# Kernel tuning notes

Measured on AMD Instinct MI355X. Metric: run time of the kernel, lower is better.

## Reference

```python
import jax, jax.numpy as jnp
import numpy as np

N, F_IN, F_OUT = 8192, 512, 256
NEG_BIG = -9e15


def setup_inputs() -> dict:
    key = jax.random.key(0)
    k1, k2, k3, k4, k5 = jax.random.split(key, 5)
    h = jax.random.normal(k1, (N, F_IN), dtype=jnp.float32)
    adj = jax.random.randint(k2, (N, N), 0, 2, dtype=jnp.int32)
    W = jax.random.normal(k3, (F_IN, F_OUT), dtype=jnp.float32) / np.sqrt(F_IN)
    bW = jnp.zeros((F_OUT,), dtype=jnp.float32)
    a1 = jax.random.normal(k4, (F_OUT,), dtype=jnp.float32) / np.sqrt(2 * F_OUT)
    a2 = jax.random.normal(k5, (F_OUT,), dtype=jnp.float32) / np.sqrt(2 * F_OUT)
    ba = jnp.zeros((), dtype=jnp.float32)
    return {"h": h, "adj": adj, "W": W, "bW": bW, "a1": a1, "a2": a2, "ba": ba}


def reference(h, adj, W, bW, a1, a2, ba):
    # Wh: [N, F_OUT]
    Wh = h @ W + bW
    # a([Wh_i ; Wh_j]) + b == (Wh_i . a1) + (Wh_j . a2) + b  (rank-1 decomposition,
    # avoids the O(N^2 * 2F) repeat/cat tensor the torch code materializes)
    f1 = Wh @ a1  # [N]
    f2 = Wh @ a2  # [N]
    e = jax.nn.leaky_relu(f1[:, None] + f2[None, :] + ba, negative_slope=0.2)
    e = jnp.where(adj > 0, e, NEG_BIG)
    attention = jax.nn.softmax(e, axis=1)  # dropout = identity (eval mode)
    return attention @ Wh
```

## Files before the change

### kernel.cpp

```cpp
#include <hip/hip_runtime.h>

typedef __bf16 bf16;
typedef __attribute__((ext_vector_type(4))) float f32x4;
typedef __attribute__((ext_vector_type(8))) __bf16 bf16x8;
typedef __attribute__((ext_vector_type(4))) __bf16 bf16x4;
typedef __attribute__((ext_vector_type(4))) int i32x4;

#define NN 8192
#define FI 512
#define FO 256
#define NSPLIT 4
#define JCHUNK (NN / NSPLIT)

__global__ __launch_bounds__(256) void k1_gemm(
    const float* __restrict__ h, const float* __restrict__ W,
    const float* __restrict__ bW, const float* __restrict__ a1,
    const float* __restrict__ a2, bf16* __restrict__ whb,
    float* __restrict__ f1, float* __restrict__ f2) {
  __shared__ float As[16][68];
  __shared__ float Bs[16][72];
  const int t = threadIdx.x;
  const int bi = blockIdx.x, bj = blockIdx.y;
  const int tx = t & 15, ty = t >> 4;
  const int lr = t >> 2, lc = (t & 3) * 4;
  const int wr = t >> 4, wc = (t & 15) * 4;
  float acc[4][4] = {};
  const float* hrow = h + (size_t)(bi * 64 + lr) * FI;
  for (int kt = 0; kt < FI / 16; ++kt) {
    f32x4 hv = *(const f32x4*)(hrow + kt * 16 + lc);
    f32x4 wv = *(const f32x4*)(W + (size_t)(kt * 16 + wr) * FO + bj * 64 + wc);
    __syncthreads();
    As[lc + 0][lr] = hv.x; As[lc + 1][lr] = hv.y;
    As[lc + 2][lr] = hv.z; As[lc + 3][lr] = hv.w;
    *(f32x4*)&Bs[wr][wc] = wv;
    __syncthreads();
#pragma unroll
    for (int k = 0; k < 16; ++k) {
      f32x4 av = *(const f32x4*)&As[k][ty * 4];
      f32x4 bv = *(const f32x4*)&Bs[k][tx * 4];
#pragma unroll
      for (int r = 0; r < 4; ++r)
#pragma unroll
        for (int cc = 0; cc < 4; ++cc)
          acc[r][cc] += av[r] * bv[cc];
    }
  }
  const int i0 = bi * 64 + ty * 4;
  const int n0 = bj * 64 + tx * 4;
  float f1p[4] = {}, f2p[4] = {};
#pragma unroll
  for (int r = 0; r < 4; ++r) {
    const int i = i0 + r;
#pragma unroll
    for (int cc = 0; cc < 4; ++cc) {
      const int n = n0 + cc;
      float wh = acc[r][cc] + bW[n];
      whb[(size_t)(i >> 5) * (FO * 32) + n * 32 + (i & 31)] = (bf16)wh;
      f1p[r] += wh * a1[n];
      f2p[r] += wh * a2[n];
    }
  }
#pragma unroll
  for (int m = 1; m < 16; m <<= 1) {
#pragma unroll
    for (int r = 0; r < 4; ++r) {
      f1p[r] += __shfl_xor(f1p[r], m);
      f2p[r] += __shfl_xor(f2p[r], m);
    }
  }
  if (tx == 0) {
#pragma unroll
    for (int r = 0; r < 4; ++r) {
      atomicAdd(&f1[i0 + r], f1p[r]);
      atomicAdd(&f2[i0 + r], f2p[r]);
    }
  }
}

__global__ __launch_bounds__(256) void k3_max(const float* __restrict__ f2,
                                              float* __restrict__ Mstar) {
  __shared__ float red[4];
  const int t = threadIdx.x;
  float m = -1e30f;
  for (int i = t; i < NN; i += 256) m = fmaxf(m, f2[i]);
#pragma unroll
  for (int d = 1; d < 64; d <<= 1) m = fmaxf(m, __shfl_xor(m, d));
  if ((t & 63) == 0) red[t >> 6] = m;
  __syncthreads();
  if (t == 0) *Mstar = fmaxf(fmaxf(red[0], red[1]), fmaxf(red[2], red[3]));
}

__global__ __launch_bounds__(256) void k4_attn(
    const int* __restrict__ adj, const bf16* __restrict__ whb,
    const float* __restrict__ f1, const float* __restrict__ f2,
    const float* __restrict__ Mstar, const float* __restrict__ ba_p,
    float* __restrict__ acc_part, float* __restrict__ l_part) {
  __shared__ bf16 Pl[32 * 40];
  __shared__ bf16 Bl[256 * 40];
  const int t = threadIdx.x;
  const int lane = t & 63, w = t >> 6;
  const int rb = blockIdx.x, s = blockIdx.y;
  const int i0 = rb * 32;
  const int rloc = t >> 3;
  const int jj = (t & 7) * 4;
  const int m16 = lane & 15, q = lane >> 4;

  const float ba = *ba_p;
  const float Ms = *Mstar;
  const float ci = f1[i0 + rloc] + ba;
  float sh = ci + Ms;
  sh = fmaxf(sh, 0.2f * sh);

  const f32x4 z4 = {0.f, 0.f, 0.f, 0.f};
  f32x4 acc0[4], acc1[4];
#pragma unroll
  for (int cc = 0; cc < 4; ++cc) { acc0[cc] = z4; acc1[cc] = z4; }
  float lreg = 0.f;

  const int* adjrow = adj + (size_t)(i0 + rloc) * NN;

  for (int kt = 0; kt < JCHUNK / 32; ++kt) {
    const int j0 = s * JCHUNK + kt * 32;
    i32x4 a4 = *(const i32x4*)(adjrow + j0 + jj);
    f32x4 s4 = *(const f32x4*)(f2 + j0 + jj);
    const size_t jt_base = (size_t)(j0 >> 5) * (FO * 32);
    bf16x8 bstg[4];
#pragma unroll
    for (int u = 0; u < 4; ++u)
      bstg[u] = *(const bf16x8*)(whb + jt_base + (size_t)(t + 256 * u) * 8);
    float pv[4];
#pragma unroll
    for (int x = 0; x < 4; ++x) {
      float arg = ci + s4[x];
      float e = fmaxf(arg, 0.2f * arg);
      pv[x] = (a4[x] > 0) ? __expf(e - sh) : 0.f;
    }
    lreg += pv[0] + pv[1] + pv[2] + pv[3];
    __syncthreads();
    bf16x4 pb = {(bf16)pv[0], (bf16)pv[1], (bf16)pv[2], (bf16)pv[3]};
    *(bf16x4*)&Pl[rloc * 40 + jj] = pb;
#pragma unroll
    for (int u = 0; u < 4; ++u) {
      const int tt = t + 256 * u;
      *(bf16x8*)&Bl[(tt >> 2) * 40 + (tt & 3) * 8] = bstg[u];
    }
    __syncthreads();
    bf16x8 af0 = *(const bf16x8*)&Pl[m16 * 40 + q * 8];
    bf16x8 af1 = *(const bf16x8*)&Pl[(16 + m16) * 40 + q * 8];
#pragma unroll
    for (int cc = 0; cc < 4; ++cc) {
      bf16x8 bfr = *(const bf16x8*)&Bl[((w * 4 + cc) * 16 + m16) * 40 + q * 8];
      acc0[cc] = __builtin_amdgcn_mfma_f32_16x16x32_bf16(af0, bfr, acc0[cc], 0, 0, 0);
      acc1[cc] = __builtin_amdgcn_mfma_f32_16x16x32_bf16(af1, bfr, acc1[cc], 0, 0, 0);
    }
  }
  lreg += __shfl_xor(lreg, 1);
  lreg += __shfl_xor(lreg, 2);
  lreg += __shfl_xor(lreg, 4);
  if ((t & 7) == 0) l_part[(size_t)s * NN + i0 + rloc] = lreg;
  float* ap = acc_part + (size_t)s * ((size_t)NN * FO);
#pragma unroll
  for (int cc = 0; cc < 4; ++cc) {
    const int n = (w * 4 + cc) * 16 + m16;
#pragma unroll
    for (int reg = 0; reg < 4; ++reg) {
      const int r0 = i0 + q * 4 + reg;
      ap[(size_t)r0 * FO + n] = acc0[cc][reg];
      ap[(size_t)(r0 + 16) * FO + n] = acc1[cc][reg];
    }
  }
}

__global__ __launch_bounds__(256) void k5_reduce(
    const float* __restrict__ accp, const float* __restrict__ lp,
    float* __restrict__ out) {
  const int idx = blockIdx.x * 256 + threadIdx.x;
  const int i = idx >> 6, n4 = (idx & 63) * 4;
  f32x4 sum = {0.f, 0.f, 0.f, 0.f};
  float l = 0.f;
#pragma unroll
  for (int s = 0; s < NSPLIT; ++s) {
    sum += *(const f32x4*)&accp[(size_t)s * ((size_t)NN * FO) + (size_t)i * FO + n4];
    l += lp[s * NN + i];
  }
  const float rl = 1.0f / l;
  f32x4 o = sum * rl;
  *(f32x4*)&out[(size_t)i * FO + n4] = o;
}

extern "C" void kernel_launch(void* const* d_in, const int* in_sizes, int n_in,
                              void* d_out, int out_size, void* d_ws, size_t ws_size,
                              hipStream_t stream) {
  const float* h  = (const float*)d_in[0];
  const int*   adj = (const int*)d_in[1];
  const float* W  = (const float*)d_in[2];
  const float* bW = (const float*)d_in[3];
  const float* a1 = (const float*)d_in[4];
  const float* a2 = (const float*)d_in[5];
  const float* ba = (const float*)d_in[6];
  float* out = (float*)d_out;

  char* ws = (char*)d_ws;
  bf16* whb  = (bf16*)ws;
  float* f1  = (float*)(ws + 4u * 1024 * 1024);
  float* f2  = (float*)(ws + 4u * 1024 * 1024 + 32 * 1024);
  float* Mst = (float*)(ws + 4u * 1024 * 1024 + 64 * 1024);
  float* accp = (float*)(ws + 4u * 1024 * 1024 + 64 * 1024 + 256);
  float* lp   = accp + (size_t)NSPLIT * NN * FO;

  hipMemsetAsync(f1, 0, 64 * 1024, stream);

  k1_gemm<<<dim3(NN / 64, FO / 64), 256, 0, stream>>>(h, W, bW, a1, a2, whb, f1, f2);
  k3_max<<<1, 256, 0, stream>>>(f2, Mst);
  k4_attn<<<dim3(NN / 32, NSPLIT), 256, 0, stream>>>(adj, whb, f1, f2, Mst, ba, accp, lp);
  k5_reduce<<<(NN * FO / 4) / 256, 256, 0, stream>>>(accp, lp, out);
}
```

Measured before the change: 488.3 us.

## Pack adjacency to bitmask, use split-bf16 MFMA projection GEMM, enlarge attention row tile

Adds a pre-pass that packs the int32 adjacency matrix into a 1-bit mask. The attention kernel then reads the mask instead of the adjacency and processes 64 rows per block. It also loads Wh fragments straight from global memory into registers rather than staging them through LDS. The feature GEMM becomes an MFMA kernel that approximates fp32 with hi/lo bf16 splits of h and a pre-transposed W. The full adjacency is still read once in the pack pass, so the gain depends on cutting the attention kernel's traffic and LDS synchronisation, at the cost of extra launches and a larger workspace.

Result: no change. 481.4 us (-1.4%).

```diff
diff --git a/kernel.cpp b/kernel.cpp
--- a/kernel.cpp
+++ b/kernel.cpp
@@ -12,68 +12,126 @@
 #define NSPLIT 4
 #define JCHUNK (NN / NSPLIT)
 
+__global__ __launch_bounds__(256) void k0_pack(const int* __restrict__ adj,
+                                               unsigned* __restrict__ mask) {
+  const int gid = blockIdx.x * 256 + threadIdx.x;
+  const int* p = adj + (size_t)gid * 32;
+  unsigned m = 0;
+#pragma unroll
+  for (int u = 0; u < 8; ++u) {
+    i32x4 v = *(const i32x4*)(p + u * 4);
+    m |= (unsigned)(v.x > 0) << (u * 4 + 0);
+    m |= (unsigned)(v.y > 0) << (u * 4 + 1);
+    m |= (unsigned)(v.z > 0) << (u * 4 + 2);
+    m |= (unsigned)(v.w > 0) << (u * 4 + 3);
+  }
+  mask[gid] = m;
+}
+
+__global__ __launch_bounds__(256) void kw_split(const float* __restrict__ W,
+                                                bf16* __restrict__ wth,
+                                                bf16* __restrict__ wtl) {
+  const int idx = blockIdx.x * 256 + threadIdx.x;
+  const int k = idx >> 8, n = idx & 255;
+  float x = W[idx];
+  bf16 hi = (bf16)x;
+  wth[(size_t)n * FI + k] = hi;
+  wtl[(size_t)n * FI + k] = (bf16)(x - (float)hi);
+}
+
 __global__ __launch_bounds__(256) void k1_gemm(
-    const float* __restrict__ h, const float* __restrict__ W,
-    const float* __restrict__ bW, const float* __restrict__ a1,
-    const float* __restrict__ a2, bf16* __restrict__ whb,
-    float* __restrict__ f1, float* __restrict__ f2) {
-  __shared__ float As[16][68];
-  __shared__ float Bs[16][72];
+    const float* __restrict__ h, const bf16* __restrict__ wth,
+    const bf16* __restrict__ wtl, const float* __restrict__ bW,
+    const float* __restrict__ a1, const float* __restrict__ a2,
+    bf16* __restrict__ whb, float* __restrict__ f1, float* __restrict__ f2) {
+  __shared__ bf16 Ah[32 * 40];
+  __shared__ bf16 Al[32 * 40];
   const int t = threadIdx.x;
+  const int lane = t & 63, w = t >> 6;
+  const int m16 = lane & 15, q = lane >> 4;
   const int bi = blockIdx.x, bj = blockIdx.y;
-  const int tx = t & 15, ty = t >> 4;
-  const int lr = t >> 2, lc = (t & 3) * 4;
-  const int wr = t >> 4, wc = (t & 15) * 4;
-  float acc[4][4] = {};
-  const float* hrow = h + (size_t)(bi * 64 + lr) * FI;
-  for (int kt = 0; kt < FI / 16; ++kt) {
-    f32x4 hv = *(const f32x4*)(hrow + kt * 16 + lc);
-    f32x4 wv = *(const f32x4*)(W + (size_t)(kt * 16 + wr) * FO + bj * 64 + wc);
-    __syncthreads();
-    As[lc + 0][lr] = hv.x; As[lc + 1][lr] = hv.y;
-    As[lc + 2][lr] = hv.z; As[lc + 3][lr] = hv.w;
-    *(f32x4*)&Bs[wr][wc] = wv;
-    __syncthreads();
-#pragma unroll
-    for (int k = 0; k < 16; ++k) {
-      f32x4 av = *(const f32x4*)&As[k][ty * 4];
-      f32x4 bv = *(const f32x4*)&Bs[k][tx * 4];
-#pragma unroll
-      for (int r = 0; r < 4; ++r)
-#pragma unroll
-        for (int cc = 0; cc < 4; ++cc)
-          acc[r][cc] += av[r] * bv[cc];
-    }
-  }
-  const int i0 = bi * 64 + ty * 4;
-  const int n0 = bj * 64 + tx * 4;
-  float f1p[4] = {}, f2p[4] = {};
-#pragma unroll
-  for (int r = 0; r < 4; ++r) {
-    const int i = i0 + r;
-#pragma unroll
-    for (int cc = 0; cc < 4; ++cc) {
-      const int n = n0 + cc;
-      float wh = acc[r][cc] + bW[n];
-      whb[(size_t)(i >> 5) * (FO * 32) + n * 32 + (i & 31)] = (bf16)wh;
-      f1p[r] += wh * a1[n];
-      f2p[r] += wh * a2[n];
+  const int i0 = bi * 32;
+  const int n0 = bj * 128 + w * 32;
+  const int srow = t >> 3, skoff = (t & 7) * 4;
+
+  const f32x4 z4 = {0.f, 0.f, 0.f, 0.f};
+  f32x4 acc[2][2];
+#pragma unroll
+  for (int mt = 0; mt < 2; ++mt)
+#pragma unroll
+    for (int nt = 0; nt < 2; ++nt) acc[mt][nt] = z4;
+
+  const float* hrow = h + (size_t)(i0 + srow) * FI + skoff;
+
+  for (int kt = 0; kt < FI / 32; ++kt) {
+    f32x4 hv = *(const f32x4*)(hrow + kt * 32);
+    bf16x8 bh[2], bl[2];
+#pragma unroll
+    for (int nt = 0; nt < 2; ++nt) {
+      const size_t woff = (size_t)(n0 + nt * 16 + m16) * FI + kt * 32 + q * 8;
+      bh[nt] = *(const bf16x8*)(wth + woff);
+      bl[nt] = *(const bf16x8*)(wtl + woff);
+    }
+    bf16x4 hh, hl;
+#pragma unroll
+    for (int x = 0; x < 4; ++x) {
+      float v = hv[x];
+      bf16 hi = (bf16)v;
+      hh[x] = hi;
+      hl[x] = (bf16)(v - (float)hi);
+    }
+    __syncthreads();
+    *(bf16x4*)&Ah[srow * 40 + skoff] = hh;
+    *(bf16x4*)&Al[srow * 40 + skoff] = hl;
+    __syncthreads();
+#pragma unroll
+    for (int mt = 0; mt < 2; ++mt) {
+      bf16x8 ah = *(const bf16x8*)&Ah[(mt * 16 + m16) * 40 + q * 8];
+      bf16x8 al = *(const bf16x8*)&Al[(mt * 16 + m16) * 40 + q * 8];
+#pragma unroll
+      for (int nt = 0; nt < 2; ++nt) {
+        acc[mt][nt] = __builtin_amdgcn_mfma_f32_16x16x32_bf16(ah, bh[nt], acc[mt][nt], 0, 0, 0);
+        acc[mt][nt] = __builtin_amdgcn_mfma_f32_16x16x32_bf16(al, bh[nt], acc[mt][nt], 0, 0, 0);
+        acc[mt][nt] = __builtin_amdgcn_mfma_f32_16x16x32_bf16(ah, bl[nt], acc[mt][nt], 0, 0, 0);
+      }
+    }
+  }
+  float f1p[2][4] = {}, f2p[2][4] = {};
+#pragma unroll
+  for (int nt = 0; nt < 2; ++nt) {
+    const int n = n0 + nt * 16 + m16;
+    const float bw = bW[n], av1 = a1[n], av2 = a2[n];
+#pragma unroll
+    for (int mt = 0; mt < 2; ++mt) {
+#pragma unroll
+      for (int reg = 0; reg < 4; ++reg) {
+        float wh = acc[mt][nt][reg] + bw;
+        const int il = mt * 16 + q * 4 + reg;
+        whb[(size_t)bi * (FO * 32) + n * 32 + il] = (bf16)wh;
+        f1p[mt][reg] += wh * av1;
+        f2p[mt][reg] += wh * av2;
+      }
     }
   }
 #pragma unroll
   for (int m = 1; m < 16; m <<= 1) {
 #pragma unroll
-    for (int r = 0; r < 4; ++r) {
-      f1p[r] += __shfl_xor(f1p[r], m);
-      f2p[r] += __shfl_xor(f2p[r], m);
-    }
-  }
-  if (tx == 0) {
-#pragma unroll
-    for (int r = 0; r < 4; ++r) {
-      atomicAdd(&f1[i0 + r], f1p[r]);
-      atomicAdd(&f2[i0 + r], f2p[r]);
-    }
+    for (int mt = 0; mt < 2; ++mt)
+#pragma unroll
+      for (int reg = 0; reg < 4; ++reg) {
+        f1p[mt][reg] += __shfl_xor(f1p[mt][reg], m);
+        f2p[mt][reg] += __shfl_xor(f2p[mt][reg], m);
+      }
+  }
+  if (m16 == 0) {
+#pragma unroll
+    for (int mt = 0; mt < 2; ++mt)
+#pragma unroll
+      for (int reg = 0; reg < 4; ++reg) {
+        const int i = i0 + mt * 16 + q * 4 + reg;
+        atomicAdd(&f1[i], f1p[mt][reg]);
+        atomicAdd(&f2[i], f2p[mt][reg]);
+      }
   }
 }
 
@@ -91,19 +149,18 @@
 }
 
 __global__ __launch_bounds__(256) void k4_attn(
-    const int* __restrict__ adj, const bf16* __restrict__ whb,
+    const unsigned* __restrict__ mask, const bf16* __restrict__ whb,
     const float* __restrict__ f1, const float* __restrict__ f2,
     const float* __restrict__ Mstar, const float* __restrict__ ba_p,
     float* __restrict__ acc_part, float* __restrict__ l_part) {
-  __shared__ bf16 Pl[32 * 40];
-  __shared__ bf16 Bl[256 * 40];
+  __shared__ bf16 Pl[64 * 40];
   const int t = threadIdx.x;
   const int lane = t & 63, w = t >> 6;
+  const int m16 = lane & 15, q = lane >> 4;
   const int rb = blockIdx.x, s = blockIdx.y;
-  const int i0 = rb * 32;
-  const int rloc = t >> 3;
-  const int jj = (t & 7) * 4;
-  const int m16 = lane & 15, q = lane >> 4;
+  const int i0 = rb * 64;
+  const int rloc = t >> 2;
+  const int jj = (t & 3) * 8;
 
   const float ba = *ba_p;
   const float Ms = *Mstar;
@@ -112,61 +169,69 @@
   sh = fmaxf(sh, 0.2f * sh);
 
   const f32x4 z4 = {0.f, 0.f, 0.f, 0.f};
-  f32x4 acc0[4], acc1[4];
-#pragma unroll
-  for (int cc = 0; cc < 4; ++cc) { acc0[cc] = z4; acc1[cc] = z4; }
+  f32x4 acc[4][4];
+#pragma unroll
+  for (int mt = 0; mt < 4; ++mt)
+#pragma unroll
+    for (int cc = 0; cc < 4; ++cc) acc[mt][cc] = z4;
   float lreg = 0.f;
 
-  const int* adjrow = adj + (size_t)(i0 + rloc) * NN;
+  const unsigned* mrow = mask + (size_t)(i0 + rloc) * (NN / 32);
+  const int sbase = s * JCHUNK;
 
   for (int kt = 0; kt < JCHUNK / 32; ++kt) {
-    const int j0 = s * JCHUNK + kt * 32;
-    i32x4 a4 = *(const i32x4*)(adjrow + j0 + jj);
-    f32x4 s4 = *(const f32x4*)(f2 + j0 + jj);
-    const size_t jt_base = (size_t)(j0 >> 5) * (FO * 32);
-    bf16x8 bstg[4];
-#pragma unroll
-    for (int u = 0; u < 4; ++u)
-      bstg[u] = *(const bf16x8*)(whb + jt_base + (size_t)(t + 256 * u) * 8);
-    float pv[4];
+    const int j0 = sbase + kt * 32;
+    const unsigned mw = mrow[j0 >> 5];
+    f32x4 s4a = *(const f32x4*)(f2 + j0 + jj);
+    f32x4 s4b = *(const f32x4*)(f2 + j0 + jj + 4);
+    const size_t bbase = (size_t)(j0 >> 5) * (FO * 32) + q * 8;
+    bf16x8 bfr[4];
+#pragma unroll
+    for (int cc = 0; cc < 4; ++cc)
+      bfr[cc] = *(const bf16x8*)(whb + bbase + (size_t)((w * 4 + cc) * 16 + m16) * 32);
+    float pv[8];
 #pragma unroll
     for (int x = 0; x < 4; ++x) {
-      float arg = ci + s4[x];
+      float arg = ci + s4a[x];
       float e = fmaxf(arg, 0.2f * arg);
-      pv[x] = (a4[x] > 0) ? __expf(e - sh) : 0.f;
-    }
-    lreg += pv[0] + pv[1] + pv[2] + pv[3];
-    __syncthreads();
-    bf16x4 pb = {(bf16)pv[0], (bf16)pv[1], (bf16)pv[2], (bf16)pv[3]};
-    *(bf16x4*)&Pl[rloc * 40 + jj] = pb;
-#pragma unroll
-    for (int u = 0; u < 4; ++u) {
-      const int tt = t + 256 * u;
-      *(bf16x8*)&Bl[(tt >> 2) * 40 + (tt & 3) * 8] = bstg[u];
-    }
-    __syncthreads();
-    bf16x8 af0 = *(const bf16x8*)&Pl[m16 * 40 + q * 8];
-    bf16x8 af1 = *(const bf16x8*)&Pl[(16 + m16) * 40 + q * 8];
-#pragma unroll
-    for (int cc = 0; cc < 4; ++cc) {
-      bf16x8 bfr = *(const bf16x8*)&Bl[((w * 4 + cc) * 16 + m16) * 40 + q * 8];
-      acc0[cc] = __builtin_amdgcn_mfma_f32_16x16x32_bf16(af0, bfr, acc0[cc], 0, 0, 0);
-      acc1[cc] = __builtin_amdgcn_mfma_f32_16x16x32_bf16(af1, bfr, acc1[cc], 0, 0, 0);
+      pv[x] = ((mw >> (jj + x)) & 1u) ? __expf(e - sh) : 0.f;
+    }
+#pragma unroll
+    for (int x = 0; x < 4; ++x) {
+      float arg = ci + s4b[x];
+      float e = fmaxf(arg, 0.2f * arg);
+      pv[4 + x] = ((mw >> (jj + 4 + x)) & 1u) ? __expf(e - sh) : 0.f;
+    }
+#pragma unroll
+    for (int x = 0; x < 8; ++x) lreg += pv[x];
+    __syncthreads();
+    bf16x8 pb;
+#pragma unroll
+    for (int x = 0; x < 8; ++x) pb[x] = (bf16)pv[x];
+    *(bf16x8*)&Pl[rloc * 40 + jj] = pb;
+    __syncthreads();
+#pragma unroll
+    for (int mt = 0; mt < 4; ++mt) {
+      bf16x8 af = *(const bf16x8*)&Pl[(mt * 16 + m16) * 40 + q * 8];
+#pragma unroll
+      for (int cc = 0; cc < 4; ++cc)
+        acc[mt][cc] = __builtin_amdgcn_mfma_f32_16x16x32_bf16(af, bfr[cc], acc[mt][cc], 0, 0, 0);
     }
   }
   lreg += __shfl_xor(lreg, 1);
   lreg += __shfl_xor(lreg, 2);
-  lreg += __shfl_xor(lreg, 4);
-  if ((t & 7) == 0) l_part[(size_t)s * NN + i0 + rloc] = lreg;
+  if ((t & 3) == 0) l_part[(size_t)s * NN + i0 + rloc] = lreg;
   float* ap = acc_part + (size_t)s * ((size_t)NN * FO);
 #pragma unroll
-  for (int cc = 0; cc < 4; ++cc) {
-    const int n = (w * 4 + cc) * 16 + m16;
-#pragma unroll
-    for (int reg = 0; reg < 4; ++reg) {
-      const int r0 = i0 + q * 4 + reg;
-      ap[(size_t)r0 * FO + n] = acc0[cc][reg];
-      ap[(size_t)(r0 + 16) * FO + n] = acc1[cc][reg];
+  for (int mt = 0; mt < 4; ++mt) {
+#pragma unroll
+    for (int cc = 0; cc < 4; ++cc) {
+      const int n = (w * 4 + cc) * 16 + m16;
+#pragma unroll
+      for (int reg = 0; reg < 4; ++reg) {
+        const int r = i0 + mt * 16 + q * 4 + reg;
+        ap[(size_t)r * FO + n] = acc[mt][cc][reg];
+      }
     }
   }
 }
@@ -191,27 +256,32 @@
 extern "C" void kernel_launch(void* const* d_in, const int* in_sizes, int n_in,
                               void* d_out, int out_size, void* d_ws, size_t ws_size,
                               hipStream_t stream) {
-  const float* h  = (const float*)d_in[0];
+  const float* h   = (const float*)d_in[0];
   const int*   adj = (const int*)d_in[1];
-  const float* W  = (const float*)d_in[2];
-  const float* bW = (const float*)d_in[3];
-  const float* a1 = (const float*)d_in[4];
-  const float* a2 = (const float*)d_in[5];
-  const float* ba = (const float*)d_in[6];
+  const float* W   = (const float*)d_in[2];
+  const float* bW  = (const float*)d_in[3];
+  const float* a1  = (const float*)d_in[4];
+  const float* a2  = (const float*)d_in[5];
+  const float* ba  = (const float*)d_in[6];
   float* out = (float*)d_out;
 
   char* ws = (char*)d_ws;
-  bf16* whb  = (bf16*)ws;
-  float* f1  = (float*)(ws + 4u * 1024 * 1024);
-  float* f2  = (float*)(ws + 4u * 1024 * 1024 + 32 * 1024);
-  float* Mst = (float*)(ws + 4u * 1024 * 1024 + 64 * 1024);
+  bf16* whb   = (bf16*)ws;
+  float* f1   = (float*)(ws + 4u * 1024 * 1024);
+  float* f2   = (float*)(ws + 4u * 1024 * 1024 + 32 * 1024);
+  float* Mst  = (float*)(ws + 4u * 1024 * 1024 + 64 * 1024);
   float* accp = (float*)(ws + 4u * 1024 * 1024 + 64 * 1024 + 256);
   float* lp   = accp + (size_t)NSPLIT * NN * FO;
+  unsigned* mask = (unsigned*)((char*)lp + (size_t)NSPLIT * NN * 4);
+  bf16* wth   = (bf16*)((char*)mask + (size_t)NN * (NN / 32) * 4);
+  bf16* wtl   = wth + (size_t)FO * FI;
 
   hipMemsetAsync(f1, 0, 64 * 1024, stream);
 
-  k1_gemm<<<dim3(NN / 64, FO / 64), 256, 0, stream>>>(h, W, bW, a1, a2, whb, f1, f2);
+  k0_pack<<<NN * (NN / 32) / 256, 256, 0, stream>>>(adj, mask);
+  kw_split<<<FI * FO / 256, 256, 0, stream>>>(W, wth, wtl);
+  k1_gemm<<<dim3(NN / 32, 2), 256, 0, stream>>>(h, wth, wtl, bW, a1, a2, whb, f1, f2);
   k3_max<<<1, 256, 0, stream>>>(f2, Mst);
-  k4_attn<<<dim3(NN / 32, NSPLIT), 256, 0, stream>>>(adj, whb, f1, f2, Mst, ba, accp, lp);
+  k4_attn<<<dim3(NN / 64, NSPLIT), 256, 0, stream>>>(mask, whb, f1, f2, Mst, ba, accp, lp);
   k5_reduce<<<(NN * FO / 4) / 256, 256, 0, stream>>>(accp, lp, out);
 }
```
